# Kernel optimization log

Hardware: AMD Instinct MI355X
Metric: run time of the kernel (lower is better)

The kernel has to match this reference:

```python
import jax, jax.numpy as jnp
import numpy as np

N = 8192          # number of nodes
IN_F = 256        # in_features
OUT_F = 128       # out_features
ALPHA = 0.2       # LeakyReLU negative slope


def setup_inputs() -> dict:
    key = jax.random.key(0)
    k1, k2, k3, k4 = jax.random.split(key, 4)
    h = jax.random.normal(k1, (N, IN_F), dtype=jnp.float32)
    adj = jax.random.randint(k2, (N, N), 0, 2, dtype=jnp.int32)  # dense 0/1 adjacency mask
    W = (jax.random.normal(k3, (IN_F, OUT_F), dtype=jnp.float32) * 0.05)   # W.weight^T
    a = (jax.random.normal(k4, (2 * OUT_F,), dtype=jnp.float32) * 0.05)    # a.weight flattened
    return {"h": h, "adj": adj, "W": W, "a": a}


def reference(h, adj, W, a):
    # Wh = self.W(h): [N, OUT_F]
    Wh = h @ W
    # Original builds an [N, N, 2F] concat tensor then projects with 'a'.
    # Equivalent math: e[i, j] = leaky_relu(Wh[i]@a1 + Wh[j]@a2)
    a1, a2 = a[:OUT_F], a[OUT_F:]
    src = Wh @ a1                                     # [N] per-source score
    dst = Wh @ a2                                     # [N] per-target score
    e = jax.nn.leaky_relu(src[:, None] + dst[None, :], negative_slope=ALPHA)  # [N, N]
    # masked softmax over neighbors (dim=1); adj==0 -> -inf
    e = jnp.where(adj == 0, -jnp.inf, e)
    attention = jax.nn.softmax(e, axis=1)             # [N, N]
    # dropout p=0 in eval-mode reference -> identity
    h_prime = attention @ Wh                          # [N, OUT_F]
    return jax.nn.elu(h_prime)                        # concat=True -> ELU
```

## Files before the change

kernel.cpp:

```cpp
#include <hip/hip_runtime.h>
#include <math.h>

#define N 8192
#define IN_F 256
#define OUT_F 128
#define ALPHA 0.2f

#define SEG 8
#define JSEG (N / SEG)
#define CHN (JSEG / 32)

typedef _Float16 f16;
typedef __attribute__((ext_vector_type(4))) float f32x4;
typedef __attribute__((ext_vector_type(8))) _Float16 f16x8;
typedef __attribute__((ext_vector_type(4))) _Float16 f16x4;
typedef __attribute__((ext_vector_type(4))) int i32x4;

__global__ __launch_bounds__(256) void k_prep(const float* __restrict__ W,
                                              f16* __restrict__ WT) {
    int idx = blockIdx.x * 256 + threadIdx.x;
    int f = idx >> 8;
    int k = idx & 255;
    WT[idx] = (f16)W[k * OUT_F + f];
}

#define HS 280
__global__ __launch_bounds__(256) void k_wh(const float* __restrict__ h,
                                            const f16* __restrict__ WT,
                                            const float* __restrict__ a,
                                            f16* __restrict__ WhT,
                                            float* __restrict__ src,
                                            float* __restrict__ dst) {
    __shared__ __align__(16) f16 hA[32][HS];
    __shared__ __align__(16) f16 outT[128][40];
    __shared__ float sred[4][32], dred[4][32];

    const int t = threadIdx.x;
    const int i0 = blockIdx.x * 32;
    const int wv = t >> 6, l = t & 63, ln = l & 15, lq = l >> 4;

    {
        const float4* hg = (const float4*)(h + (size_t)i0 * IN_F);
#pragma unroll
        for (int it = 0; it < 8; ++it) {
            int idx = t + it * 256;
            int r = idx >> 6;
            int c4 = (idx & 63) * 4;
            float4 v = hg[idx];
            f16x4 p = { (f16)v.x, (f16)v.y, (f16)v.z, (f16)v.w };
            *(f16x4*)&hA[r][c4] = p;
        }
    }
    __syncthreads();

    f32x4 acc00 = {0.f,0.f,0.f,0.f}, acc01 = {0.f,0.f,0.f,0.f};
    f32x4 acc10 = {0.f,0.f,0.f,0.f}, acc11 = {0.f,0.f,0.f,0.f};
    const int f0 = 32 * wv;

#pragma unroll
    for (int ks = 0; ks < 8; ++ks) {
        const int k0 = 32 * ks + 8 * lq;
        f16x8 a0 = *(const f16x8*)&hA[ln][k0];
        f16x8 a1 = *(const f16x8*)&hA[16 + ln][k0];
        f16x8 b0 = *(const f16x8*)(WT + (size_t)(f0 + ln) * IN_F + k0);
        f16x8 b1 = *(const f16x8*)(WT + (size_t)(f0 + 16 + ln) * IN_F + k0);
        acc00 = __builtin_amdgcn_mfma_f32_16x16x32_f16(a0, b0, acc00, 0, 0, 0);
        acc01 = __builtin_amdgcn_mfma_f32_16x16x32_f16(a0, b1, acc01, 0, 0, 0);
        acc10 = __builtin_amdgcn_mfma_f32_16x16x32_f16(a1, b0, acc10, 0, 0, 0);
        acc11 = __builtin_amdgcn_mfma_f32_16x16x32_f16(a1, b1, acc11, 0, 0, 0);
    }

    const float a1c0 = a[f0 + ln],      a2c0 = a[128 + f0 + ln];
    const float a1c1 = a[f0 + 16 + ln], a2c1 = a[128 + f0 + 16 + ln];
    float sp[8], dp[8];
#pragma unroll
    for (int i = 0; i < 8; ++i) { sp[i] = 0.f; dp[i] = 0.f; }

#pragma unroll
    for (int hh = 0; hh < 2; ++hh) {
        f32x4 v0 = hh ? acc10 : acc00;
        f32x4 v1 = hh ? acc11 : acc01;
        f16x4 p0, p1;
#pragma unroll
        for (int rg = 0; rg < 4; ++rg) {
            sp[hh * 4 + rg] += v0[rg] * a1c0 + v1[rg] * a1c1;
            dp[hh * 4 + rg] += v0[rg] * a2c0 + v1[rg] * a2c1;
            p0[rg] = (f16)v0[rg];
            p1[rg] = (f16)v1[rg];
        }
        *(f16x4*)&outT[f0 + ln][16 * hh + 4 * lq] = p0;
        *(f16x4*)&outT[f0 + 16 + ln][16 * hh + 4 * lq] = p1;
    }
#pragma unroll
    for (int i = 0; i < 8; ++i) {
        float s = sp[i], d = dp[i];
        s += __shfl_down(s, 8, 16); d += __shfl_down(d, 8, 16);
        s += __shfl_down(s, 4, 16); d += __shfl_down(d, 4, 16);
        s += __shfl_down(s, 2, 16); d += __shfl_down(d, 2, 16);
        s += __shfl_down(s, 1, 16); d += __shfl_down(d, 1, 16);
        if (ln == 0) {
            int row = 16 * (i >> 2) + 4 * lq + (i & 3);
            sred[wv][row] = s;
            dred[wv][row] = d;
        }
    }
    __syncthreads();
    if (t < 32) {
        src[i0 + t] = sred[0][t] + sred[1][t] + sred[2][t] + sred[3][t];
        dst[i0 + t] = dred[0][t] + dred[1][t] + dred[2][t] + dred[3][t];
    }
    {
        const int col = t & 127, g = t >> 7;
        f16x8 q0 = *(const f16x8*)&outT[col][16 * g];
        f16x8 q1 = *(const f16x8*)&outT[col][16 * g + 8];
        *(f16x8*)(WhT + (size_t)col * N + i0 + 16 * g) = q0;
        *(f16x8*)(WhT + (size_t)col * N + i0 + 16 * g + 8) = q1;
    }
}

__global__ __launch_bounds__(256) void k_attn(const int* __restrict__ adj,
                                              const f16* __restrict__ WhT,
                                              const float* __restrict__ src,
                                              const float* __restrict__ dst,
                                              float* __restrict__ part,
                                              float* __restrict__ lpPart) {
    const int t = threadIdx.x;
    const int wv = t >> 6, l = t & 63, ln = l & 15, lq = l >> 4;
    const int bid = blockIdx.x;
    const int s  = bid & (SEG - 1);
    const int rg = bid >> 3;
    const int R0 = rg * 128 + wv * 32;
    const int jb = s * JSEG;

    const float src0 = src[R0 + ln],      src1 = src[R0 + 16 + ln];
    const float csh0 = fabsf(src0) + 4.0f, csh1 = fabsf(src1) + 4.0f;

    const int*   __restrict__ ar0 = adj + (size_t)(R0 + ln) * N + jb + 8 * lq;
    const int*   __restrict__ ar1 = adj + (size_t)(R0 + 16 + ln) * N + jb + 8 * lq;
    const float* __restrict__ dp  = dst + jb + 8 * lq;
    const f16*   __restrict__ Bp  = WhT + (size_t)ln * N + jb + 8 * lq;

    f32x4 acc0[8], acc1[8];
#pragma unroll
    for (int i = 0; i < 8; ++i) {
        acc0[i] = (f32x4){0.f, 0.f, 0.f, 0.f};
        acc1[i] = (f32x4){0.f, 0.f, 0.f, 0.f};
    }
    float lp0 = 0.f, lp1 = 0.f;

    i32x4 aA00, aA01, aA10, aA11, aB00, aB01, aB10, aB11;
    f32x4 dA0, dA1, dB0, dB1;

#define ISSUE(c, A00, A01, A10, A11, D0, D1)                                   \
    {                                                                          \
        const int o = (c) * 32;                                                \
        A00 = __builtin_nontemporal_load((const i32x4*)(ar0 + o));             \
        A01 = __builtin_nontemporal_load((const i32x4*)(ar0 + o + 4));         \
        A10 = __builtin_nontemporal_load((const i32x4*)(ar1 + o));             \
        A11 = __builtin_nontemporal_load((const i32x4*)(ar1 + o + 4));         \
        D0  = *(const f32x4*)(dp + o);                                         \
        D1  = *(const f32x4*)(dp + o + 4);                                     \
    }

    auto cw = [&](const i32x4& A00, const i32x4& A01, const i32x4& A10, const i32x4& A11,
                  const f32x4& D0, const f32x4& D1, f16x8& w0, f16x8& w1) {
#pragma unroll
        for (int k = 0; k < 4; ++k) {
            float e, lk, v;
            e = src0 + D0[k]; lk = fmaf(0.4f, fabsf(e), 0.6f * e);
            v = A00[k] ? __expf(lk - csh0) : 0.f; lp0 += v; w0[k] = (f16)v;
            e = src0 + D1[k]; lk = fmaf(0.4f, fabsf(e), 0.6f * e);
            v = A01[k] ? __expf(lk - csh0) : 0.f; lp0 += v; w0[4 + k] = (f16)v;
            e = src1 + D0[k]; lk = fmaf(0.4f, fabsf(e), 0.6f * e);
            v = A10[k] ? __expf(lk - csh1) : 0.f; lp1 += v; w1[k] = (f16)v;
            e = src1 + D1[k]; lk = fmaf(0.4f, fabsf(e), 0.6f * e);
            v = A11[k] ? __expf(lk - csh1) : 0.f; lp1 += v; w1[4 + k] = (f16)v;
        }
    };

    ISSUE(0, aA00, aA01, aA10, aA11, dA0, dA1);
    ISSUE(1, aB00, aB01, aB10, aB11, dB0, dB1);

    for (int c = 0; c < CHN; c += 2) {
        {
            const f16* bp = Bp + c * 32;
            f16x8 b[8];
#pragma unroll
            for (int ft = 0; ft < 8; ++ft)
                b[ft] = *(const f16x8*)(bp + (size_t)(16 * ft) * N);
            f16x8 w0, w1;
            cw(aA00, aA01, aA10, aA11, dA0, dA1, w0, w1);
            if (c + 2 < CHN) ISSUE(c + 2, aA00, aA01, aA10, aA11, dA0, dA1);
#pragma unroll
            for (int ft = 0; ft < 8; ++ft) {
                acc0[ft] = __builtin_amdgcn_mfma_f32_16x16x32_f16(w0, b[ft], acc0[ft], 0, 0, 0);
                acc1[ft] = __builtin_amdgcn_mfma_f32_16x16x32_f16(w1, b[ft], acc1[ft], 0, 0, 0);
            }
        }
        {
            const f16* bp = Bp + (c + 1) * 32;
            f16x8 b[8];
#pragma unroll
            for (int ft = 0; ft < 8; ++ft)
                b[ft] = *(const f16x8*)(bp + (size_t)(16 * ft) * N);
            f16x8 w0, w1;
            cw(aB00, aB01, aB10, aB11, dB0, dB1, w0, w1);
            if (c + 3 < CHN) ISSUE(c + 3, aB00, aB01, aB10, aB11, dB0, dB1);
#pragma unroll
            for (int ft = 0; ft < 8; ++ft) {
                acc0[ft] = __builtin_amdgcn_mfma_f32_16x16x32_f16(w0, b[ft], acc0[ft], 0, 0, 0);
                acc1[ft] = __builtin_amdgcn_mfma_f32_16x16x32_f16(w1, b[ft], acc1[ft], 0, 0, 0);
            }
        }
    }
#undef ISSUE

    lp0 += __shfl_xor(lp0, 16); lp0 += __shfl_xor(lp0, 32);
    lp1 += __shfl_xor(lp1, 16); lp1 += __shfl_xor(lp1, 32);
    if (l < 16) {
        lpPart[(size_t)s * N + R0 + ln]      = lp0;
        lpPart[(size_t)s * N + R0 + 16 + ln] = lp1;
    }

    float* __restrict__ pp = part + ((size_t)s * N + R0) * OUT_F;
#pragma unroll
    for (int ft = 0; ft < 8; ++ft)
#pragma unroll
        for (int r = 0; r < 4; ++r) {
            pp[(size_t)(4 * lq + r) * OUT_F + 16 * ft + ln]        = acc0[ft][r];
            pp[(size_t)(16 + 4 * lq + r) * OUT_F + 16 * ft + ln]   = acc1[ft][r];
        }
}

__global__ __launch_bounds__(256) void k_comb(const float* __restrict__ part,
                                              const float* __restrict__ lpPart,
                                              float* __restrict__ out) {
    const int idx = blockIdx.x * 256 + threadIdx.x;
    const int row = idx >> 5;
    const int c4  = idx & 31;

    float lsum = 0.f;
#pragma unroll
    for (int s = 0; s < SEG; ++s) lsum += lpPart[(size_t)s * N + row];

    f32x4 v = {0.f, 0.f, 0.f, 0.f};
#pragma unroll
    for (int s = 0; s < SEG; ++s)
        v += *(const f32x4*)(part + ((size_t)s * N + row) * OUT_F + c4 * 4);

    const float inv = 1.0f / lsum;
    f32x4 r;
#pragma unroll
    for (int k = 0; k < 4; ++k) {
        float hp = v[k] * inv;
        r[k] = hp > 0.f ? hp : expm1f(hp);
    }
    *(f32x4*)(out + (size_t)row * OUT_F + c4 * 4) = r;
}

extern "C" void kernel_launch(void* const* d_in, const int* in_sizes, int n_in,
                              void* d_out, int out_size, void* d_ws, size_t ws_size,
                              hipStream_t stream) {
    const float* h   = (const float*)d_in[0];
    const int*   adj = (const int*)d_in[1];
    const float* W   = (const float*)d_in[2];
    const float* a   = (const float*)d_in[3];
    float* out = (float*)d_out;

    f16*   WT  = (f16*)d_ws;
    f16*   WhT = (f16*)((char*)d_ws + (1 << 16));
    float* src = (float*)((char*)WhT + (size_t)OUT_F * N * sizeof(f16));
    float* dst = src + N;
    float* lpP = dst + N;
    float* part = (float*)((char*)d_ws + (8u << 20));

    k_prep<<<128, 256, 0, stream>>>(W, WT);
    k_wh<<<N / 32, 256, 0, stream>>>(h, WT, a, WhT, src, dst);
    k_attn<<<(N / 128) * SEG, 256, 0, stream>>>(adj, WhT, src, dst, part, lpP);
    k_comb<<<(N * OUT_F / 4) / 256, 256, 0, stream>>>(part, lpP, out);
}
```

Measured before the change: 424.1 us.

## Fuse split-K combine into attention kernel via in-block LDS reduction

New measurement: 450.9 us. +6.3%, slower.

```diff
diff --git a/kernel.cpp b/kernel.cpp
--- a/kernel.cpp
+++ b/kernel.cpp
@@ -118,19 +118,23 @@
     }
 }
 
-__global__ __launch_bounds__(256) void k_attn(const int* __restrict__ adj,
-                                              const f16* __restrict__ WhT,
-                                              const float* __restrict__ src,
-                                              const float* __restrict__ dst,
-                                              float* __restrict__ part,
-                                              float* __restrict__ lpPart) {
+#define ALS 132
+__global__ __launch_bounds__(512, 2) void k_attn(const int* __restrict__ adj,
+                                                 const f16* __restrict__ WhT,
+                                                 const float* __restrict__ src,
+                                                 const float* __restrict__ dst,
+                                                 float* __restrict__ out) {
+    __shared__ __align__(16) float accL[32][ALS];
+    __shared__ float lpL[32];
+
     const int t = threadIdx.x;
     const int wv = t >> 6, l = t & 63, ln = l & 15, lq = l >> 4;
-    const int bid = blockIdx.x;
-    const int s  = bid & (SEG - 1);
-    const int rg = bid >> 3;
-    const int R0 = rg * 128 + wv * 32;
-    const int jb = s * JSEG;
+    const int R0 = blockIdx.x * 32;
+    const int jb = wv * JSEG;
+
+    for (int i = t; i < 32 * ALS; i += 512) ((float*)accL)[i] = 0.f;
+    if (t < 32) lpL[t] = 0.f;
+    __syncthreads();
 
     const float src0 = src[R0 + ln],      src1 = src[R0 + 16 + ln];
     const float csh0 = fabsf(src0) + 4.0f, csh1 = fabsf(src1) + 4.0f;
@@ -218,44 +222,37 @@
     lp0 += __shfl_xor(lp0, 16); lp0 += __shfl_xor(lp0, 32);
     lp1 += __shfl_xor(lp1, 16); lp1 += __shfl_xor(lp1, 32);
     if (l < 16) {
-        lpPart[(size_t)s * N + R0 + ln]      = lp0;
-        lpPart[(size_t)s * N + R0 + 16 + ln] = lp1;
-    }
-
-    float* __restrict__ pp = part + ((size_t)s * N + R0) * OUT_F;
+        atomicAdd(&lpL[ln], lp0);
+        atomicAdd(&lpL[16 + ln], lp1);
+    }
+
 #pragma unroll
     for (int ft = 0; ft < 8; ++ft)
 #pragma unroll
         for (int r = 0; r < 4; ++r) {
-            pp[(size_t)(4 * lq + r) * OUT_F + 16 * ft + ln]        = acc0[ft][r];
-            pp[(size_t)(16 + 4 * lq + r) * OUT_F + 16 * ft + ln]   = acc1[ft][r];
-        }
-}
-
-__global__ __launch_bounds__(256) void k_comb(const float* __restrict__ part,
-                                              const float* __restrict__ lpPart,
-                                              float* __restrict__ out) {
-    const int idx = blockIdx.x * 256 + threadIdx.x;
-    const int row = idx >> 5;
-    const int c4  = idx & 31;
-
-    float lsum = 0.f;
-#pragma unroll
-    for (int s = 0; s < SEG; ++s) lsum += lpPart[(size_t)s * N + row];
-
-    f32x4 v = {0.f, 0.f, 0.f, 0.f};
-#pragma unroll
-    for (int s = 0; s < SEG; ++s)
-        v += *(const f32x4*)(part + ((size_t)s * N + row) * OUT_F + c4 * 4);
-
-    const float inv = 1.0f / lsum;
-    f32x4 r;
-#pragma unroll
-    for (int k = 0; k < 4; ++k) {
-        float hp = v[k] * inv;
-        r[k] = hp > 0.f ? hp : expm1f(hp);
-    }
-    *(f32x4*)(out + (size_t)row * OUT_F + c4 * 4) = r;
+            atomicAdd(&accL[4 * lq + r][16 * ft + ln],      acc0[ft][r]);
+            atomicAdd(&accL[16 + 4 * lq + r][16 * ft + ln], acc1[ft][r]);
+        }
+    __syncthreads();
+
+    {
+        const int row = t >> 4;
+        const int c0  = (t & 15) * 8;
+        const float inv = 1.0f / lpL[row];
+        f32x4 v0 = *(const f32x4*)&accL[row][c0];
+        f32x4 v1 = *(const f32x4*)&accL[row][c0 + 4];
+        f32x4 r0, r1;
+#pragma unroll
+        for (int k = 0; k < 4; ++k) {
+            float h0 = v0[k] * inv;
+            float h1 = v1[k] * inv;
+            r0[k] = h0 > 0.f ? h0 : expm1f(h0);
+            r1[k] = h1 > 0.f ? h1 : expm1f(h1);
+        }
+        float* op = out + (size_t)(R0 + row) * OUT_F + c0;
+        *(f32x4*)op = r0;
+        *(f32x4*)(op + 4) = r1;
+    }
 }
 
 extern "C" void kernel_launch(void* const* d_in, const int* in_sizes, int n_in,
@@ -271,11 +268,8 @@
     f16*   WhT = (f16*)((char*)d_ws + (1 << 16));
     float* src = (float*)((char*)WhT + (size_t)OUT_F * N * sizeof(f16));
     float* dst = src + N;
-    float* lpP = dst + N;
-    float* part = (float*)((char*)d_ws + (8u << 20));
 
     k_prep<<<128, 256, 0, stream>>>(W, WT);
     k_wh<<<N / 32, 256, 0, stream>>>(h, WT, a, WhT, src, dst);
-    k_attn<<<(N / 128) * SEG, 256, 0, stream>>>(adj, WhT, src, dst, part, lpP);
-    k_comb<<<(N * OUT_F / 4) / 256, 256, 0, stream>>>(part, lpP, out);
-}
+    k_attn<<<N / 32, 512, 0, stream>>>(adj, WhT, src, dst, out);
+}
```

## Fuse split-K combine into attention kernel and deepen adjacency prefetch to four stages

Applied to the files above, without the earlier changes.

After: 532.8 us. +25.6%, slower.

```diff
diff --git a/kernel.cpp b/kernel.cpp
--- a/kernel.cpp
+++ b/kernel.cpp
@@ -17,11 +17,13 @@
 typedef __attribute__((ext_vector_type(4))) int i32x4;
 
 __global__ __launch_bounds__(256) void k_prep(const float* __restrict__ W,
-                                              f16* __restrict__ WT) {
+                                              f16* __restrict__ WT,
+                                              int* __restrict__ cnt) {
     int idx = blockIdx.x * 256 + threadIdx.x;
     int f = idx >> 8;
     int k = idx & 255;
     WT[idx] = (f16)W[k * OUT_F + f];
+    if (idx < 64) cnt[idx] = 0;
 }
 
 #define HS 280
@@ -123,7 +125,11 @@
                                               const float* __restrict__ src,
                                               const float* __restrict__ dst,
                                               float* __restrict__ part,
-                                              float* __restrict__ lpPart) {
+                                              float* __restrict__ lpPart,
+                                              int* __restrict__ cnt,
+                                              float* __restrict__ out) {
+    __shared__ int lastF;
+
     const int t = threadIdx.x;
     const int wv = t >> 6, l = t & 63, ln = l & 15, lq = l >> 4;
     const int bid = blockIdx.x;
@@ -148,18 +154,15 @@
     }
     float lp0 = 0.f, lp1 = 0.f;
 
-    i32x4 aA00, aA01, aA10, aA11, aB00, aB01, aB10, aB11;
-    f32x4 dA0, dA1, dB0, dB1;
-
-#define ISSUE(c, A00, A01, A10, A11, D0, D1)                                   \
+    i32x4 a0_[4], a1_[4], a2_[4], a3_[4];
+
+#define ISSUE(c, S)                                                            \
     {                                                                          \
         const int o = (c) * 32;                                                \
-        A00 = __builtin_nontemporal_load((const i32x4*)(ar0 + o));             \
-        A01 = __builtin_nontemporal_load((const i32x4*)(ar0 + o + 4));         \
-        A10 = __builtin_nontemporal_load((const i32x4*)(ar1 + o));             \
-        A11 = __builtin_nontemporal_load((const i32x4*)(ar1 + o + 4));         \
-        D0  = *(const f32x4*)(dp + o);                                         \
-        D1  = *(const f32x4*)(dp + o + 4);                                     \
+        a0_[S] = __builtin_nontemporal_load((const i32x4*)(ar0 + o));          \
+        a1_[S] = __builtin_nontemporal_load((const i32x4*)(ar0 + o + 4));      \
+        a2_[S] = __builtin_nontemporal_load((const i32x4*)(ar1 + o));          \
+        a3_[S] = __builtin_nontemporal_load((const i32x4*)(ar1 + o + 4));      \
     }
 
     auto cw = [&](const i32x4& A00, const i32x4& A01, const i32x4& A10, const i32x4& A11,
@@ -178,40 +181,31 @@
         }
     };
 
-    ISSUE(0, aA00, aA01, aA10, aA11, dA0, dA1);
-    ISSUE(1, aB00, aB01, aB10, aB11, dB0, dB1);
-
-    for (int c = 0; c < CHN; c += 2) {
-        {
-            const f16* bp = Bp + c * 32;
-            f16x8 b[8];
-#pragma unroll
-            for (int ft = 0; ft < 8; ++ft)
-                b[ft] = *(const f16x8*)(bp + (size_t)(16 * ft) * N);
-            f16x8 w0, w1;
-            cw(aA00, aA01, aA10, aA11, dA0, dA1, w0, w1);
-            if (c + 2 < CHN) ISSUE(c + 2, aA00, aA01, aA10, aA11, dA0, dA1);
-#pragma unroll
-            for (int ft = 0; ft < 8; ++ft) {
-                acc0[ft] = __builtin_amdgcn_mfma_f32_16x16x32_f16(w0, b[ft], acc0[ft], 0, 0, 0);
-                acc1[ft] = __builtin_amdgcn_mfma_f32_16x16x32_f16(w1, b[ft], acc1[ft], 0, 0, 0);
-            }
-        }
-        {
-            const f16* bp = Bp + (c + 1) * 32;
-            f16x8 b[8];
-#pragma unroll
-            for (int ft = 0; ft < 8; ++ft)
-                b[ft] = *(const f16x8*)(bp + (size_t)(16 * ft) * N);
-            f16x8 w0, w1;
-            cw(aB00, aB01, aB10, aB11, dB0, dB1, w0, w1);
-            if (c + 3 < CHN) ISSUE(c + 3, aB00, aB01, aB10, aB11, dB0, dB1);
-#pragma unroll
-            for (int ft = 0; ft < 8; ++ft) {
-                acc0[ft] = __builtin_amdgcn_mfma_f32_16x16x32_f16(w0, b[ft], acc0[ft], 0, 0, 0);
-                acc1[ft] = __builtin_amdgcn_mfma_f32_16x16x32_f16(w1, b[ft], acc1[ft], 0, 0, 0);
-            }
-        }
+    auto step = [&](int c, int S) {
+        const f16* bp = Bp + c * 32;
+        f16x8 b[8];
+#pragma unroll
+        for (int ft = 0; ft < 8; ++ft)
+            b[ft] = *(const f16x8*)(bp + (size_t)(16 * ft) * N);
+        f32x4 D0 = *(const f32x4*)(dp + c * 32);
+        f32x4 D1 = *(const f32x4*)(dp + c * 32 + 4);
+        f16x8 w0, w1;
+        cw(a0_[S], a1_[S], a2_[S], a3_[S], D0, D1, w0, w1);
+        if (c + 4 < CHN) ISSUE(c + 4, S);
+#pragma unroll
+        for (int ft = 0; ft < 8; ++ft) {
+            acc0[ft] = __builtin_amdgcn_mfma_f32_16x16x32_f16(w0, b[ft], acc0[ft], 0, 0, 0);
+            acc1[ft] = __builtin_amdgcn_mfma_f32_16x16x32_f16(w1, b[ft], acc1[ft], 0, 0, 0);
+        }
+    };
+
+    ISSUE(0, 0); ISSUE(1, 1); ISSUE(2, 2); ISSUE(3, 3);
+
+    for (int c = 0; c < CHN; c += 4) {
+        step(c + 0, 0);
+        step(c + 1, 1);
+        step(c + 2, 2);
+        step(c + 3, 3);
     }
 #undef ISSUE
 
@@ -230,32 +224,45 @@
             pp[(size_t)(4 * lq + r) * OUT_F + 16 * ft + ln]        = acc0[ft][r];
             pp[(size_t)(16 + 4 * lq + r) * OUT_F + 16 * ft + ln]   = acc1[ft][r];
         }
-}
-
-__global__ __launch_bounds__(256) void k_comb(const float* __restrict__ part,
-                                              const float* __restrict__ lpPart,
-                                              float* __restrict__ out) {
-    const int idx = blockIdx.x * 256 + threadIdx.x;
-    const int row = idx >> 5;
-    const int c4  = idx & 31;
-
-    float lsum = 0.f;
-#pragma unroll
-    for (int s = 0; s < SEG; ++s) lsum += lpPart[(size_t)s * N + row];
-
-    f32x4 v = {0.f, 0.f, 0.f, 0.f};
-#pragma unroll
-    for (int s = 0; s < SEG; ++s)
-        v += *(const f32x4*)(part + ((size_t)s * N + row) * OUT_F + c4 * 4);
-
-    const float inv = 1.0f / lsum;
-    f32x4 r;
-#pragma unroll
-    for (int k = 0; k < 4; ++k) {
-        float hp = v[k] * inv;
-        r[k] = hp > 0.f ? hp : expm1f(hp);
-    }
-    *(f32x4*)(out + (size_t)row * OUT_F + c4 * 4) = r;
+
+    __syncthreads();
+    if (t == 0) {
+        __threadfence();
+        lastF = (atomicAdd(&cnt[rg], 1) == SEG - 1);
+    }
+    __syncthreads();
+    if (!lastF) return;
+    __threadfence();
+
+    {
+        const int row = rg * 128 + (t >> 1);
+        const int c0  = (t & 1) * 64;
+        float lsum = 0.f;
+#pragma unroll
+        for (int sg = 0; sg < SEG; ++sg) lsum += lpPart[(size_t)sg * N + row];
+        const float inv = 1.0f / lsum;
+
+        f32x4 v[16];
+#pragma unroll
+        for (int q = 0; q < 16; ++q) v[q] = (f32x4){0.f, 0.f, 0.f, 0.f};
+#pragma unroll
+        for (int sg = 0; sg < SEG; ++sg) {
+            const float* p = part + ((size_t)sg * N + row) * OUT_F + c0;
+#pragma unroll
+            for (int q = 0; q < 16; ++q) v[q] += *(const f32x4*)(p + 4 * q);
+        }
+        float* op = out + (size_t)row * OUT_F + c0;
+#pragma unroll
+        for (int q = 0; q < 16; ++q) {
+            f32x4 r;
+#pragma unroll
+            for (int k = 0; k < 4; ++k) {
+                float hp = v[q][k] * inv;
+                r[k] = hp > 0.f ? hp : expm1f(hp);
+            }
+            *(f32x4*)(op + 4 * q) = r;
+        }
+    }
 }
 
 extern "C" void kernel_launch(void* const* d_in, const int* in_sizes, int n_in,
@@ -273,9 +280,9 @@
     float* dst = src + N;
     float* lpP = dst + N;
     float* part = (float*)((char*)d_ws + (8u << 20));
-
-    k_prep<<<128, 256, 0, stream>>>(W, WT);
+    int*   cnt  = (int*)((char*)d_ws + (46u << 20));
+
+    k_prep<<<128, 256, 0, stream>>>(W, WT, cnt);
     k_wh<<<N / 32, 256, 0, stream>>>(h, WT, a, WhT, src, dst);
-    k_attn<<<(N / 128) * SEG, 256, 0, stream>>>(adj, WhT, src, dst, part, lpP);
-    k_comb<<<(N * OUT_F / 4) / 256, 256, 0, stream>>>(part, lpP, out);
-}
+    k_attn<<<(N / 128) * SEG, 256, 0, stream>>>(adj, WhT, src, dst, part, lpP, cnt, out);
+}
```
